# Optimization experiments

Measured on AMD Instinct MI355X. Metric: run time of the kernel, lower is better.

The kernel has to match this reference:

```python
import jax, jax.numpy as jnp
import numpy as np

N_NODES = 100000


def sage_conv(x, edge_index, W_l, b_l, W_r):
    # PyG SAGEConv (mean aggr): out = lin_l(mean_j x_j) + lin_r(x_i)
    src = edge_index[0]
    dst = edge_index[1]
    msg_sum = jax.ops.segment_sum(x[src], dst, num_segments=N_NODES)  # [N, d]
    deg = jax.ops.segment_sum(jnp.ones(src.shape[0], dtype=x.dtype), dst,
                              num_segments=N_NODES)  # [N]
    mean = msg_sum / jnp.maximum(deg, 1.0)[:, None]
    return mean @ W_l + b_l + x @ W_r


def setup_inputs() -> dict:
    key = jax.random.key(0)
    ks = jax.random.split(key, 8)
    d_in, hidden, d_out = 128, 256, 128
    n_edges = 1600000
    x = jax.random.normal(ks[0], (N_NODES, d_in), dtype=jnp.float32)
    edge_index = jax.random.randint(ks[1], (2, n_edges), 0, N_NODES, dtype=jnp.int64)
    s1 = 1.0 / np.sqrt(d_in)
    s2 = 1.0 / np.sqrt(hidden)
    return {
        "x": x,
        "edge_index": edge_index,
        "W_l1": jax.random.uniform(ks[2], (d_in, hidden), jnp.float32, -s1, s1),
        "b_l1": jnp.zeros((hidden,), jnp.float32),
        "W_r1": jax.random.uniform(ks[3], (d_in, hidden), jnp.float32, -s1, s1),
        "W_l2": jax.random.uniform(ks[4], (hidden, d_out), jnp.float32, -s2, s2),
        "b_l2": jnp.zeros((d_out,), jnp.float32),
        "W_r2": jax.random.uniform(ks[5], (hidden, d_out), jnp.float32, -s2, s2),
    }


def reference(x, edge_index, W_l1, b_l1, W_r1, W_l2, b_l2, W_r2):
    h = jax.nn.relu(sage_conv(x, edge_index, W_l1, b_l1, W_r1))
    return sage_conv(h, edge_index, W_l2, b_l2, W_r2)
```

## Files before the change

kernel.cpp:

```cpp
#include <hip/hip_runtime.h>

#define N_NODES 100000
#define NPAD 100096
#define NBLK 391

using bf16x8 = __attribute__((ext_vector_type(8))) short;
using f32x4  = __attribute__((ext_vector_type(4))) float;

__device__ inline short f2bf(float f) {
    unsigned int u = __float_as_uint(f);
    unsigned int r = (u + 0x7FFFu + ((u >> 16) & 1u)) >> 16;
    return (short)r;
}
__device__ inline float bf2f_lo(unsigned int w) { return __uint_as_float(w << 16); }
__device__ inline float bf2f_hi(unsigned int w) { return __uint_as_float(w & 0xFFFF0000u); }

__global__ __launch_bounds__(256)
void cbuck_kernel(const int* __restrict__ dst, int* __restrict__ bucket_cnt, int E) {
    __shared__ int cnt[NBLK];
    const int tid = threadIdx.x;
    for (int i = tid; i < NBLK; i += 256) cnt[i] = 0;
    __syncthreads();
    const int e0 = blockIdx.x * 4096;
    #pragma unroll
    for (int k = 0; k < 16; ++k) {
        int e = e0 + k * 256 + tid;
        if (e < E) atomicAdd(&cnt[dst[e] >> 8], 1);
    }
    __syncthreads();
    for (int i = tid; i < NBLK; i += 256)
        if (cnt[i]) atomicAdd(&bucket_cnt[i], cnt[i]);
}

__global__ void scan391_kernel(const int* __restrict__ bucket_cnt, int* __restrict__ bucket_base,
                               int* __restrict__ bucket_cursor, int* __restrict__ offsets) {
    __shared__ int s[512];
    int t = threadIdx.x;
    int v = (t < NBLK) ? bucket_cnt[t] : 0;
    s[t] = v;
    __syncthreads();
    #pragma unroll
    for (int off = 1; off < 512; off <<= 1) {
        int u = (t >= off) ? s[t - off] : 0;
        __syncthreads();
        s[t] += u;
        __syncthreads();
    }
    if (t < NBLK) {
        int excl = s[t] - v;
        bucket_base[t] = excl;
        bucket_cursor[t] = excl;
    }
    if (t == NBLK - 1) {
        bucket_base[NBLK] = s[t];
        offsets[N_NODES] = s[t];
    }
}

__global__ __launch_bounds__(256)
void bin_kernel(const int* __restrict__ src, const int* __restrict__ dst,
                int* __restrict__ bucket_cursor, unsigned int* __restrict__ bin, int E) {
    __shared__ int cnt[NBLK];
    __shared__ int base_l[NBLK];
    const int tid = threadIdx.x;
    const int e0 = blockIdx.x * 4096;
    for (int i = tid; i < NBLK; i += 256) cnt[i] = 0;
    __syncthreads();
    int myb[16]; unsigned myv[16];
    #pragma unroll
    for (int k = 0; k < 16; ++k) {
        int e = e0 + k * 256 + tid;
        if (e < E) {
            int d = dst[e];
            myb[k] = d >> 8;
            myv[k] = (unsigned)src[e] | ((unsigned)(d & 255) << 20);
            atomicAdd(&cnt[myb[k]], 1);
        } else myb[k] = -1;
    }
    __syncthreads();
    for (int i = tid; i < NBLK; i += 256) {
        int c = cnt[i];
        base_l[i] = c ? atomicAdd(&bucket_cursor[i], c) : 0;
        cnt[i] = 0;
    }
    __syncthreads();
    #pragma unroll
    for (int k = 0; k < 16; ++k) {
        if (myb[k] >= 0) {
            int slot = base_l[myb[k]] + atomicAdd(&cnt[myb[k]], 1);
            bin[slot] = myv[k];
        }
    }
}

__global__ __launch_bounds__(256)
void place_kernel(const unsigned int* __restrict__ bin, const int* __restrict__ bucket_base,
                  int* __restrict__ offsets, int* __restrict__ sorted) {
    __shared__ int cnt[256];
    __shared__ int cur[256];
    __shared__ int wsum[4];
    const int b = blockIdx.x, tid = threadIdx.x;
    const int lane = tid & 63, wave = tid >> 6;
    const int s = bucket_base[b];
    const int e = bucket_base[b + 1];
    cnt[tid] = 0;
    __syncthreads();
    for (int i = s + tid; i < e; i += 256) atomicAdd(&cnt[bin[i] >> 20], 1);
    __syncthreads();
    int v = cnt[tid];
    int x = v;
    #pragma unroll
    for (int off = 1; off < 64; off <<= 1) {
        int t = __shfl_up(x, off, 64);
        if (lane >= off) x += t;
    }
    if (lane == 63) wsum[wave] = x;
    __syncthreads();
    int woff = 0;
    #pragma unroll
    for (int w = 0; w < 4; ++w) if (w < wave) woff += wsum[w];
    int excl = s + woff + x - v;
    cur[tid] = excl;
    int node = b * 256 + tid;
    if (node < N_NODES) offsets[node] = excl;
    __syncthreads();
    for (int i = s + tid; i < e; i += 256) {
        unsigned w = bin[i];
        int p = atomicAdd(&cur[w >> 20], 1);
        sorted[p] = (int)(w & 0xFFFFFu);
    }
}

__global__ void cast_x_kernel(const float* __restrict__ x, short* __restrict__ xrow,
                              short* __restrict__ xpack) {
    int t = blockIdx.x * 256 + threadIdx.x;
    if (t >= N_NODES * 16) return;
    int row = t >> 4;
    int kc = (t & 15) << 3;
    const float4 v0 = *(const float4*)(x + (size_t)row * 128 + kc);
    const float4 v1 = *(const float4*)(x + (size_t)row * 128 + kc + 4);
    __align__(16) short s[8] = {f2bf(v0.x), f2bf(v0.y), f2bf(v0.z), f2bf(v0.w),
                                f2bf(v1.x), f2bf(v1.y), f2bf(v1.z), f2bf(v1.w)};
    *(int4*)(xrow + (size_t)row * 128 + kc) = *(const int4*)s;
    size_t pidx = ((size_t)(row >> 4) * 16 + (kc >> 3)) * 128 + (size_t)(row & 15) * 8;
    *(int4*)(xpack + pidx) = *(const int4*)s;
}

__global__ void pack_w_kernel(const float* __restrict__ W, short* __restrict__ P,
                              int K, int NC) {
    int t = blockIdx.x * 256 + threadIdx.x;
    if (t >= K * NC) return;
    int k = t / NC, c = t % NC;
    P[((size_t)(c >> 4) * (K >> 3) + (k >> 3)) * 128 + (size_t)(c & 15) * 8 + (k & 7)] = f2bf(W[t]);
}

template<int MODE>
__global__ __launch_bounds__(256)
void aggregate128_kernel(const short* __restrict__ feat, const int* __restrict__ offsets,
                         const int* __restrict__ srcs,
                         short* __restrict__ outpack, float* __restrict__ outf) {
    int node = blockIdx.x * 4 + (threadIdx.x >> 6);
    if (node >= N_NODES) return;
    const int lane = threadIdx.x & 63;
    const int g = lane >> 4, p = lane & 15;
    const int s = offsets[node], e = offsets[node + 1];
    const float inv = 1.0f / (float)max(e - s, 1);
    float acc[8] = {0.f, 0.f, 0.f, 0.f, 0.f, 0.f, 0.f, 0.f};
    for (int j = s + g; j < e; j += 8) {
        const int j2 = j + 4;
        const bool h2 = (j2 < e);
        const int i0 = srcs[j];
        const int i1 = h2 ? srcs[j2] : i0;
        const uint4 w0 = *(const uint4*)(feat + (size_t)i0 * 128 + p * 8);
        const uint4 w1 = *(const uint4*)(feat + (size_t)i1 * 128 + p * 8);
        acc[0] += bf2f_lo(w0.x); acc[1] += bf2f_hi(w0.x);
        acc[2] += bf2f_lo(w0.y); acc[3] += bf2f_hi(w0.y);
        acc[4] += bf2f_lo(w0.z); acc[5] += bf2f_hi(w0.z);
        acc[6] += bf2f_lo(w0.w); acc[7] += bf2f_hi(w0.w);
        if (h2) {
            acc[0] += bf2f_lo(w1.x); acc[1] += bf2f_hi(w1.x);
            acc[2] += bf2f_lo(w1.y); acc[3] += bf2f_hi(w1.y);
            acc[4] += bf2f_lo(w1.z); acc[5] += bf2f_hi(w1.z);
            acc[6] += bf2f_lo(w1.w); acc[7] += bf2f_hi(w1.w);
        }
    }
    #pragma unroll
    for (int t = 0; t < 8; ++t) acc[t] += __shfl_xor(acc[t], 16, 64);
    #pragma unroll
    for (int t = 0; t < 8; ++t) acc[t] += __shfl_xor(acc[t], 32, 64);
    if (g != 0) return;
    if (MODE == 0) {
        __align__(16) short r[8];
        #pragma unroll
        for (int t = 0; t < 8; ++t) r[t] = f2bf(acc[t] * inv);
        size_t pidx = ((size_t)(node >> 4) * 16 + p) * 128 + (size_t)(node & 15) * 8;
        *(int4*)(outpack + pidx) = *(const int4*)r;
    } else {
        float* o = outf + (size_t)node * 128 + p * 8;
        float4 q0 = *(const float4*)o;
        float4 q1 = *(const float4*)(o + 4);
        q0.x += acc[0] * inv; q0.y += acc[1] * inv; q0.z += acc[2] * inv; q0.w += acc[3] * inv;
        q1.x += acc[4] * inv; q1.y += acc[5] * inv; q1.z += acc[6] * inv; q1.w += acc[7] * inv;
        *(float4*)o = q0;
        *(float4*)(o + 4) = q1;
    }
}

__global__ __launch_bounds__(256)
void gemm1_kernel(const short* __restrict__ A0, const short* __restrict__ A1,
                  const short* __restrict__ B0, const short* __restrict__ B1,
                  const float* __restrict__ bias, short* __restrict__ opack) {
    constexpr int KB = 16, KS = 4, S = 8;
    __shared__ float sC[4][32][132];
    const int tid = threadIdx.x, wave = tid >> 6, lane = tid & 63;
    const int lhi = lane >> 4, llo = lane & 15;
    const int rowBase = blockIdx.x * 256 + wave * 64;
    const int colBase = blockIdx.y * 128;
    const int rowTile = rowBase >> 4, colTile = colBase >> 4;

    f32x4 acc[4][8];
    #pragma unroll
    for (int i = 0; i < 4; ++i)
        #pragma unroll
        for (int j = 0; j < 8; ++j)
            #pragma unroll
            for (int r = 0; r < 4; ++r) acc[i][j][r] = 0.f;

    bf16x8 a[4];
    #pragma unroll
    for (int i = 0; i < 4; ++i)
        a[i] = *(const bf16x8*)(A0 + ((size_t)(rowTile + i) * KB + lhi) * 128 + (size_t)llo * 8);

    #pragma unroll
    for (int s = 0; s < S; ++s) {
        const short* B = (s >= KS) ? B1 : B0;
        const int kb = (s - (s >= KS ? KS : 0)) * 4 + lhi;
        bf16x8 b[8];
        #pragma unroll
        for (int j = 0; j < 8; ++j)
            b[j] = *(const bf16x8*)(B + ((size_t)(colTile + j) * KB + kb) * 128 + (size_t)llo * 8);
        bf16x8 an[4];
        if (s + 1 < S) {
            const int s1 = s + 1;
            const short* A = (s1 >= KS) ? A1 : A0;
            const int kb1 = (s1 - (s1 >= KS ? KS : 0)) * 4 + lhi;
            #pragma unroll
            for (int i = 0; i < 4; ++i)
                an[i] = *(const bf16x8*)(A + ((size_t)(rowTile + i) * KB + kb1) * 128 + (size_t)llo * 8);
        }
        #pragma unroll
        for (int i = 0; i < 4; ++i)
            #pragma unroll
            for (int j = 0; j < 8; ++j)
                acc[i][j] = __builtin_amdgcn_mfma_f32_16x16x32_bf16(a[i], b[j], acc[i][j], 0, 0, 0);
        if (s + 1 < S) {
            #pragma unroll
            for (int i = 0; i < 4; ++i) a[i] = an[i];
        }
    }

    #pragma unroll
    for (int j = 0; j < 8; ++j) {
        float bv = bias[colBase + j * 16 + llo];
        #pragma unroll
        for (int i = 0; i < 4; ++i)
            #pragma unroll
            for (int r = 0; r < 4; ++r)
                acc[i][j][r] = fmaxf(acc[i][j][r] + bv, 0.f);
    }

    #pragma unroll
    for (int half = 0; half < 2; ++half) {
        #pragma unroll
        for (int i2 = 0; i2 < 2; ++i2) {
            const int i = half * 2 + i2;
            #pragma unroll
            for (int j = 0; j < 8; ++j)
                #pragma unroll
                for (int r = 0; r < 4; ++r)
                    sC[wave][i2 * 16 + lhi * 4 + r][j * 16 + llo] = acc[i][j][r];
        }
        #pragma unroll
        for (int it = 0; it < 8; ++it) {
            const int r = it * 4 + (lane >> 4);
            const int c = (lane & 15) * 8;
            const int grow = rowBase + half * 32 + r;
            if (grow < N_NODES) {
                float4 v0 = *(const float4*)&sC[wave][r][c];
                float4 v1 = *(const float4*)&sC[wave][r][c + 4];
                __align__(16) short sv[8] = {f2bf(v0.x), f2bf(v0.y), f2bf(v0.z), f2bf(v0.w),
                                             f2bf(v1.x), f2bf(v1.y), f2bf(v1.z), f2bf(v1.w)};
                size_t pidx = ((size_t)(grow >> 4) * 32 + ((colBase + c) >> 3)) * 128
                            + (size_t)(grow & 15) * 8;
                *(int4*)(opack + pidx) = *(const int4*)sv;
            }
        }
    }
}

__global__ __launch_bounds__(256)
void gemm2_kernel(const short* __restrict__ A, const short* __restrict__ B0,
                  const short* __restrict__ B1, const float* __restrict__ bias,
                  short* __restrict__ prow, float* __restrict__ qf32) {
    constexpr int KB = 32, S = 8;
    __shared__ float sC[4][32][68];
    const int tid = threadIdx.x, wave = tid >> 6, lane = tid & 63;
    const int lhi = lane >> 4, llo = lane & 15;
    const int rowBase = blockIdx.x * 256 + wave * 64;
    const int colBase = blockIdx.y * 64;
    const int rowTile = rowBase >> 4, colTile = colBase >> 4;

    f32x4 accp[4][4], accq[4][4];
    #pragma unroll
    for (int i = 0; i < 4; ++i)
        #pragma unroll
        for (int j = 0; j < 4; ++j)
            #pragma unroll
            for (int r = 0; r < 4; ++r) { accp[i][j][r] = 0.f; accq[i][j][r] = 0.f; }

    bf16x8 a[4];
    #pragma unroll
    for (int i = 0; i < 4; ++i)
        a[i] = *(const bf16x8*)(A + ((size_t)(rowTile + i) * KB + lhi) * 128 + (size_t)llo * 8);

    #pragma unroll
    for (int s = 0; s < S; ++s) {
        const int kb = s * 4 + lhi;
        bf16x8 b0[4], b1[4];
        #pragma unroll
        for (int j = 0; j < 4; ++j) {
            b0[j] = *(const bf16x8*)(B0 + ((size_t)(colTile + j) * KB + kb) * 128 + (size_t)llo * 8);
            b1[j] = *(const bf16x8*)(B1 + ((size_t)(colTile + j) * KB + kb) * 128 + (size_t)llo * 8);
        }
        bf16x8 an[4];
        if (s + 1 < S) {
            const int kb1 = (s + 1) * 4 + lhi;
            #pragma unroll
            for (int i = 0; i < 4; ++i)
                an[i] = *(const bf16x8*)(A + ((size_t)(rowTile + i) * KB + kb1) * 128 + (size_t)llo * 8);
        }
        #pragma unroll
        for (int i = 0; i < 4; ++i)
            #pragma unroll
            for (int j = 0; j < 4; ++j) {
                accp[i][j] = __builtin_amdgcn_mfma_f32_16x16x32_bf16(a[i], b0[j], accp[i][j], 0, 0, 0);
                accq[i][j] = __builtin_amdgcn_mfma_f32_16x16x32_bf16(a[i], b1[j], accq[i][j], 0, 0, 0);
            }
        if (s + 1 < S) {
            #pragma unroll
            for (int i = 0; i < 4; ++i) a[i] = an[i];
        }
    }

    #pragma unroll
    for (int half = 0; half < 2; ++half) {
        #pragma unroll
        for (int i2 = 0; i2 < 2; ++i2) {
            const int i = half * 2 + i2;
            #pragma unroll
            for (int j = 0; j < 4; ++j)
                #pragma unroll
                for (int r = 0; r < 4; ++r)
                    sC[wave][i2 * 16 + lhi * 4 + r][j * 16 + llo] = accp[i][j][r];
        }
        #pragma unroll
        for (int it = 0; it < 4; ++it) {
            const int r = it * 8 + (lane >> 3);
            const int c = (lane & 7) * 8;
            const int grow = rowBase + half * 32 + r;
            if (grow < N_NODES) {
                float4 v0 = *(const float4*)&sC[wave][r][c];
                float4 v1 = *(const float4*)&sC[wave][r][c + 4];
                __align__(16) short sv[8] = {f2bf(v0.x), f2bf(v0.y), f2bf(v0.z), f2bf(v0.w),
                                             f2bf(v1.x), f2bf(v1.y), f2bf(v1.z), f2bf(v1.w)};
                *(int4*)(prow + (size_t)grow * 128 + colBase + c) = *(const int4*)sv;
            }
        }
    }

    #pragma unroll
    for (int j = 0; j < 4; ++j) {
        float bv = bias[colBase + j * 16 + llo];
        #pragma unroll
        for (int i = 0; i < 4; ++i)
            #pragma unroll
            for (int r = 0; r < 4; ++r) accq[i][j][r] += bv;
    }
    #pragma unroll
    for (int half = 0; half < 2; ++half) {
        #pragma unroll
        for (int i2 = 0; i2 < 2; ++i2) {
            const int i = half * 2 + i2;
            #pragma unroll
            for (int j = 0; j < 4; ++j)
                #pragma unroll
                for (int r = 0; r < 4; ++r)
                    sC[wave][i2 * 16 + lhi * 4 + r][j * 16 + llo] = accq[i][j][r];
        }
        #pragma unroll
        for (int it = 0; it < 4; ++it) {
            const int r = it * 8 + (lane >> 3);
            const int c = (lane & 7) * 8;
            const int grow = rowBase + half * 32 + r;
            if (grow < N_NODES) {
                float4 v0 = *(const float4*)&sC[wave][r][c];
                float4 v1 = *(const float4*)&sC[wave][r][c + 4];
                *(float4*)(qf32 + (size_t)grow * 128 + colBase + c) = v0;
                *(float4*)(qf32 + (size_t)grow * 128 + colBase + c + 4) = v1;
            }
        }
    }
}

extern "C" void kernel_launch(void* const* d_in, const int* in_sizes, int n_in,
                              void* d_out, int out_size, void* d_ws, size_t ws_size,
                              hipStream_t stream) {
    const float* x   = (const float*)d_in[0];
    const int*   ei  = (const int*)d_in[1];
    const float* Wl1 = (const float*)d_in[2];
    const float* b1  = (const float*)d_in[3];
    const float* Wr1 = (const float*)d_in[4];
    const float* Wl2 = (const float*)d_in[5];
    const float* b2  = (const float*)d_in[6];
    const float* Wr2 = (const float*)d_in[7];
    const int E = in_sizes[1] / 2;
    const int* src = ei;
    const int* dst = ei + E;

    short* h_pack = (short*)d_ws;
    short* agg1p  = h_pack + (size_t)NPAD * 256;
    short* x_row  = agg1p  + (size_t)NPAD * 128;
    short* x_pack = x_row  + (size_t)NPAD * 128;
    short* p_row  = x_pack + (size_t)NPAD * 128;
    short* wl1p   = p_row  + (size_t)NPAD * 128;
    short* wr1p   = wl1p + 32768;
    short* wl2p   = wr1p + 32768;
    short* wr2p   = wl2p + 32768;
    int* bucket_cnt    = (int*)(wr2p + 32768);
    int* bucket_base   = bucket_cnt + NBLK + 1;
    int* bucket_cursor = bucket_base + NBLK + 1;
    int* offsets       = bucket_cursor + NBLK + 1;
    unsigned int* bin  = (unsigned int*)(offsets + N_NODES + 1);
    int* sorted        = (int*)(bin + E);

    const int nbin = (E + 4095) / 4096;

    hipMemsetAsync(bucket_cnt, 0, (NBLK + 1) * sizeof(int), stream);
    cbuck_kernel<<<nbin, 256, 0, stream>>>(dst, bucket_cnt, E);
    scan391_kernel<<<1, 512, 0, stream>>>(bucket_cnt, bucket_base, bucket_cursor, offsets);
    bin_kernel<<<nbin, 256, 0, stream>>>(src, dst, bucket_cursor, bin, E);
    place_kernel<<<NBLK, 256, 0, stream>>>(bin, bucket_base, offsets, sorted);

    cast_x_kernel<<<(N_NODES * 16 + 255) / 256, 256, 0, stream>>>(x, x_row, x_pack);
    pack_w_kernel<<<128, 256, 0, stream>>>(Wl1, wl1p, 128, 256);
    pack_w_kernel<<<128, 256, 0, stream>>>(Wr1, wr1p, 128, 256);
    pack_w_kernel<<<128, 256, 0, stream>>>(Wl2, wl2p, 256, 128);
    pack_w_kernel<<<128, 256, 0, stream>>>(Wr2, wr2p, 256, 128);

    aggregate128_kernel<0><<<N_NODES / 4, 256, 0, stream>>>(x_row, offsets, sorted, agg1p, nullptr);
    gemm1_kernel<<<dim3(NPAD / 256, 2), 256, 0, stream>>>(agg1p, x_pack, wl1p, wr1p, b1, h_pack);

    gemm2_kernel<<<dim3(NPAD / 256, 2), 256, 0, stream>>>(h_pack, wl2p, wr2p, b2, p_row, (float*)d_out);
    aggregate128_kernel<1><<<N_NODES / 4, 256, 0, stream>>>(p_row, offsets, sorted, nullptr, (float*)d_out);
}
```

Baseline: 304.3 us.

## Fuse prep launches, deepen gather unroll, and remap GEMM blocks across XCDs

Merges the x cast and the four weight-pack kernels into one prep kernel, which removes four launches. Unrolls the aggregate gather loop to four independent edge loads per lane group so more memory requests are in flight. Remaps the GEMM grid so each XCD gets a contiguous range of row blocks, with both column halves of a row block on the same XCD, to improve L2 reuse of the A tiles. The remap adds a few idle blocks that exit early, and the per-load predicates raise branch overhead.

```diff
diff --git a/kernel.cpp b/kernel.cpp
--- a/kernel.cpp
+++ b/kernel.cpp
@@ -14,6 +14,16 @@
 }
 __device__ inline float bf2f_lo(unsigned int w) { return __uint_as_float(w << 16); }
 __device__ inline float bf2f_hi(unsigned int w) { return __uint_as_float(w & 0xFFFF0000u); }
+
+__device__ inline bool xcd_map(int bid, int& row, int& col) {
+    const int RP = (NBLK + 7) / 8;
+    const int xcd = bid & 7;
+    const int i = bid >> 3;
+    row = xcd * RP + (i >> 1);
+    col = i & 1;
+    return row < NBLK;
+}
+#define GEMM_GRID (8 * 2 * ((NBLK + 7) / 8))
 
 __global__ __launch_bounds__(256)
 void cbuck_kernel(const int* __restrict__ dst, int* __restrict__ bucket_cnt, int E) {
@@ -131,28 +141,43 @@
     }
 }
 
-__global__ void cast_x_kernel(const float* __restrict__ x, short* __restrict__ xrow,
-                              short* __restrict__ xpack) {
+__global__ __launch_bounds__(256)
+void prep_kernel(const float* __restrict__ x, short* __restrict__ xrow, short* __restrict__ xpack,
+                 const float* __restrict__ Wl1, const float* __restrict__ Wr1,
+                 const float* __restrict__ Wl2, const float* __restrict__ Wr2,
+                 short* __restrict__ wl1p, short* __restrict__ wr1p,
+                 short* __restrict__ wl2p, short* __restrict__ wr2p) {
     int t = blockIdx.x * 256 + threadIdx.x;
-    if (t >= N_NODES * 16) return;
-    int row = t >> 4;
-    int kc = (t & 15) << 3;
-    const float4 v0 = *(const float4*)(x + (size_t)row * 128 + kc);
-    const float4 v1 = *(const float4*)(x + (size_t)row * 128 + kc + 4);
-    __align__(16) short s[8] = {f2bf(v0.x), f2bf(v0.y), f2bf(v0.z), f2bf(v0.w),
-                                f2bf(v1.x), f2bf(v1.y), f2bf(v1.z), f2bf(v1.w)};
-    *(int4*)(xrow + (size_t)row * 128 + kc) = *(const int4*)s;
-    size_t pidx = ((size_t)(row >> 4) * 16 + (kc >> 3)) * 128 + (size_t)(row & 15) * 8;
-    *(int4*)(xpack + pidx) = *(const int4*)s;
-}
-
-__global__ void pack_w_kernel(const float* __restrict__ W, short* __restrict__ P,
-                              int K, int NC) {
-    int t = blockIdx.x * 256 + threadIdx.x;
-    if (t >= K * NC) return;
-    int k = t / NC, c = t % NC;
-    P[((size_t)(c >> 4) * (K >> 3) + (k >> 3)) * 128 + (size_t)(c & 15) * 8 + (k & 7)] = f2bf(W[t]);
-}
+    if (t < N_NODES * 16) {
+        int row = t >> 4;
+        int kc = (t & 15) << 3;
+        const float4 v0 = *(const float4*)(x + (size_t)row * 128 + kc);
+        const float4 v1 = *(const float4*)(x + (size_t)row * 128 + kc + 4);
+        __align__(16) short s[8] = {f2bf(v0.x), f2bf(v0.y), f2bf(v0.z), f2bf(v0.w),
+                                    f2bf(v1.x), f2bf(v1.y), f2bf(v1.z), f2bf(v1.w)};
+        *(int4*)(xrow + (size_t)row * 128 + kc) = *(const int4*)s;
+        size_t pidx = ((size_t)(row >> 4) * 16 + (kc >> 3)) * 128 + (size_t)(row & 15) * 8;
+        *(int4*)(xpack + pidx) = *(const int4*)s;
+        return;
+    }
+    int u = t - N_NODES * 16;
+    if (u >= 4 * 32768) return;
+    const int w = u >> 15;
+    const int t2 = u & 32767;
+    const float* W; short* P; int K, NC;
+    if (w == 0)      { W = Wl1; P = wl1p; K = 128; NC = 256; }
+    else if (w == 1) { W = Wr1; P = wr1p; K = 128; NC = 256; }
+    else if (w == 2) { W = Wl2; P = wl2p; K = 256; NC = 128; }
+    else             { W = Wr2; P = wr2p; K = 256; NC = 128; }
+    int k = t2 / NC, c = t2 % NC;
+    P[((size_t)(c >> 4) * (K >> 3) + (k >> 3)) * 128 + (size_t)(c & 15) * 8 + (k & 7)] = f2bf(W[t2]);
+}
+
+#define ADD8(A, W) \
+    A[0] += bf2f_lo(W.x); A[1] += bf2f_hi(W.x); \
+    A[2] += bf2f_lo(W.y); A[3] += bf2f_hi(W.y); \
+    A[4] += bf2f_lo(W.z); A[5] += bf2f_hi(W.z); \
+    A[6] += bf2f_lo(W.w); A[7] += bf2f_hi(W.w);
 
 template<int MODE>
 __global__ __launch_bounds__(256)
@@ -166,22 +191,22 @@
     const int s = offsets[node], e = offsets[node + 1];
     const float inv = 1.0f / (float)max(e - s, 1);
     float acc[8] = {0.f, 0.f, 0.f, 0.f, 0.f, 0.f, 0.f, 0.f};
-    for (int j = s + g; j < e; j += 8) {
-        const int j2 = j + 4;
-        const bool h2 = (j2 < e);
-        const int i0 = srcs[j];
-        const int i1 = h2 ? srcs[j2] : i0;
-        const uint4 w0 = *(const uint4*)(feat + (size_t)i0 * 128 + p * 8);
-        const uint4 w1 = *(const uint4*)(feat + (size_t)i1 * 128 + p * 8);
-        acc[0] += bf2f_lo(w0.x); acc[1] += bf2f_hi(w0.x);
-        acc[2] += bf2f_lo(w0.y); acc[3] += bf2f_hi(w0.y);
-        acc[4] += bf2f_lo(w0.z); acc[5] += bf2f_hi(w0.z);
-        acc[6] += bf2f_lo(w0.w); acc[7] += bf2f_hi(w0.w);
-        if (h2) {
-            acc[0] += bf2f_lo(w1.x); acc[1] += bf2f_hi(w1.x);
-            acc[2] += bf2f_lo(w1.y); acc[3] += bf2f_hi(w1.y);
-            acc[4] += bf2f_lo(w1.z); acc[5] += bf2f_hi(w1.z);
-            acc[6] += bf2f_lo(w1.w); acc[7] += bf2f_hi(w1.w);
+    for (int j = s + g; j < e; j += 16) {
+        const int ja = j + 4, jb = j + 8, jc = j + 12;
+        const bool ha = ja < e, hb = jb < e, hc = jc < e;
+        const uint4 w0 = *(const uint4*)(feat + (size_t)srcs[j] * 128 + p * 8);
+        ADD8(acc, w0)
+        if (ha) {
+            const uint4 w1 = *(const uint4*)(feat + (size_t)srcs[ja] * 128 + p * 8);
+            ADD8(acc, w1)
+        }
+        if (hb) {
+            const uint4 w2 = *(const uint4*)(feat + (size_t)srcs[jb] * 128 + p * 8);
+            ADD8(acc, w2)
+        }
+        if (hc) {
+            const uint4 w3 = *(const uint4*)(feat + (size_t)srcs[jc] * 128 + p * 8);
+            ADD8(acc, w3)
         }
     }
     #pragma unroll
@@ -212,10 +237,12 @@
                   const float* __restrict__ bias, short* __restrict__ opack) {
     constexpr int KB = 16, KS = 4, S = 8;
     __shared__ float sC[4][32][132];
+    int rowBlk, colHalf;
+    if (!xcd_map(blockIdx.x, rowBlk, colHalf)) return;
     const int tid = threadIdx.x, wave = tid >> 6, lane = tid & 63;
     const int lhi = lane >> 4, llo = lane & 15;
-    const int rowBase = blockIdx.x * 256 + wave * 64;
-    const int colBase = blockIdx.y * 128;
+    const int rowBase = rowBlk * 256 + wave * 64;
+    const int colBase = colHalf * 128;
     const int rowTile = rowBase >> 4, colTile = colBase >> 4;
 
     f32x4 acc[4][8];
@@ -304,10 +331,12 @@
                   short* __restrict__ prow, float* __restrict__ qf32) {
     constexpr int KB = 32, S = 8;
     __shared__ float sC[4][32][68];
+    int rowBlk, colHalf;
+    if (!xcd_map(blockIdx.x, rowBlk, colHalf)) return;
     const int tid = threadIdx.x, wave = tid >> 6, lane = tid & 63;
     const int lhi = lane >> 4, llo = lane & 15;
-    const int rowBase = blockIdx.x * 256 + wave * 64;
-    const int colBase = blockIdx.y * 64;
+    const int rowBase = rowBlk * 256 + wave * 64;
+    const int colBase = colHalf * 64;
     const int rowTile = rowBase >> 4, colTile = colBase >> 4;
 
     f32x4 accp[4][4], accq[4][4];
@@ -451,15 +480,12 @@
     bin_kernel<<<nbin, 256, 0, stream>>>(src, dst, bucket_cursor, bin, E);
     place_kernel<<<NBLK, 256, 0, stream>>>(bin, bucket_base, offsets, sorted);
 
-    cast_x_kernel<<<(N_NODES * 16 + 255) / 256, 256, 0, stream>>>(x, x_row, x_pack);
-    pack_w_kernel<<<128, 256, 0, stream>>>(Wl1, wl1p, 128, 256);
-    pack_w_kernel<<<128, 256, 0, stream>>>(Wr1, wr1p, 128, 256);
-    pack_w_kernel<<<128, 256, 0, stream>>>(Wl2, wl2p, 256, 128);
-    pack_w_kernel<<<128, 256, 0, stream>>>(Wr2, wr2p, 256, 128);
+    prep_kernel<<<(N_NODES * 16 + 4 * 32768 + 255) / 256, 256, 0, stream>>>(
+        x, x_row, x_pack, Wl1, Wr1, Wl2, Wr2, wl1p, wr1p, wl2p, wr2p);
 
     aggregate128_kernel<0><<<N_NODES / 4, 256, 0, stream>>>(x_row, offsets, sorted, agg1p, nullptr);
-    gemm1_kernel<<<dim3(NPAD / 256, 2), 256, 0, stream>>>(agg1p, x_pack, wl1p, wr1p, b1, h_pack);
-
-    gemm2_kernel<<<dim3(NPAD / 256, 2), 256, 0, stream>>>(h_pack, wl2p, wr2p, b2, p_row, (float*)d_out);
+    gemm1_kernel<<<GEMM_GRID, 256, 0, stream>>>(agg1p, x_pack, wl1p, wr1p, b1, h_pack);
+
+    gemm2_kernel<<<GEMM_GRID, 256, 0, stream>>>(h_pack, wl2p, wr2p, b2, p_row, (float*)d_out);
     aggregate128_kernel<1><<<N_NODES / 4, 256, 0, stream>>>(p_row, offsets, sorted, nullptr, (float*)d_out);
 }
```

Result: no change. 305.0 us (+0.2%).
